# Kernel tuning notes

Measured on AMD Instinct MI355X. Metric: run time of the kernel, lower is better.

Reference implementation:

```python
import jax, jax.numpy as jnp
import numpy as np

B, T, N = 256, 50, 32          # graphs per batch, timesteps, nodes per scene graph
FIN, HG, HR, HFC = 16, 64, 64, 128  # gnn in, gnn hidden, gnn out (== HG, shared LayerNorm), gru hidden
DS, DTG, OST, OCA = 32, 32, 8, 8    # sensor dim, target dim, stimuli classes, cause classes


def _ln(x, g, b, eps=1e-5):
    m = jnp.mean(x, axis=-1, keepdims=True)
    v = jnp.var(x, axis=-1, keepdims=True)
    return (x - m) * jax.lax.rsqrt(v + eps) * g + b


def _gru_seq(x, Wi, Wh, bi, bh):
    # x: [B, T, Din] -> [B, T, H]; PyTorch GRU gate order (r, z, n)
    xp = x @ Wi + bi  # precompute input projections for all timesteps
    H = Wh.shape[0]
    h0 = jnp.zeros((x.shape[0], H), x.dtype)
    def step(h, xt):
        gh = h @ Wh + bh
        ir, iz, ig = jnp.split(xt, 3, axis=-1)
        hr, hz, hg = jnp.split(gh, 3, axis=-1)
        r = jax.nn.sigmoid(ir + hr)
        z = jax.nn.sigmoid(iz + hz)
        n = jnp.tanh(ig + r * hg)
        hn = (1.0 - z) * n + z * h
        return hn, hn
    _, ys = jax.lax.scan(step, h0, jnp.swapaxes(xp, 0, 1))
    return jnp.swapaxes(ys, 0, 1)


def _glorot(key, shape):
    s = jnp.sqrt(2.0 / (shape[0] + shape[-1]))
    return jax.random.normal(key, shape, jnp.float32) * s


def setup_inputs() -> dict:
    key = jax.random.key(0)
    ks = jax.random.split(key, 24)
    inp = {
        'feat': jax.random.normal(ks[0], (B, T, N, FIN), jnp.float32),
        'sensor': jax.random.normal(ks[1], (B, T, DS), jnp.float32),
        'target': jax.random.normal(ks[2], (B, T, DTG), jnp.float32),
        'adj': jax.random.randint(ks[3], (B, T, N, N), 0, 2, jnp.int32),
        'W_g1': _glorot(ks[4], (FIN, HG)), 'b_g1': jnp.zeros((HG,)),
        'W_g3': _glorot(ks[5], (HG, HR)), 'b_g3': jnp.zeros((HR,)),
        'ln_g_g': jnp.ones((HG,)), 'ln_g_b': jnp.zeros((HG,)),
    }
    for i, (sfx, din) in enumerate([('G', HR), ('S', DS), ('T', DTG)]):
        inp['Wi' + sfx] = _glorot(ks[6 + 2 * i], (din, 3 * HFC))
        inp['Wh' + sfx] = _glorot(ks[7 + 2 * i], (HFC, 3 * HFC))
        inp['bi' + sfx] = jnp.zeros((3 * HFC,))
        inp['bh' + sfx] = jnp.zeros((3 * HFC,))
    inp['W_fc1'] = _glorot(ks[12], (3 * HFC, HFC)); inp['b_fc1'] = jnp.zeros((HFC,))
    inp['ln_fc_g'] = jnp.ones((HFC,)); inp['ln_fc_b'] = jnp.zeros((HFC,))
    inp['W_st'] = _glorot(ks[13], (HFC, OST)); inp['b_st'] = jnp.zeros((OST,))
    inp['W_ca'] = _glorot(ks[14], (HFC, OCA)); inp['b_ca'] = jnp.zeros((OCA,))
    return inp


def reference(feat, sensor, target, W_g1, b_g1, W_g3, b_g3, ln_g_g, ln_g_b,
              WiG, WhG, biG, bhG, WiS, WhS, biS, bhS, WiT, WhT, biT, bhT,
              W_fc1, b_fc1, ln_fc_g, ln_fc_b, W_st, b_st, W_ca, b_ca, adj):
    # Batched mean-aggregation GNN (self-loops avoid zero in-degree), fused over all B*T graphs.
    adj_f = adj.astype(jnp.float32) + jnp.eye(N, dtype=jnp.float32)
    deg = jnp.sum(adj_f, axis=-1, keepdims=True)  # [B,T,N,1]
    def gnn(h, W, b):
        agg = jnp.einsum('btij,btjf->btif', adj_f, h) / deg
        return jax.nn.relu(_ln(agg @ W + b, ln_g_g, ln_g_b))  # linear -> norm -> relu (dropout=0)
    h1 = gnn(feat, W_g1, b_g1)   # gnn1c
    h2 = gnn(h1, W_g3, b_g3)     # gnn3c
    graph_seq = h2[:, :, 0, :]   # hG[0]: node-0 readout per (graph, timestep) -> [B,T,HR]
    gG = _gru_seq(graph_seq, WiG, WhG, biG, bhG)
    gS = _gru_seq(sensor, WiS, WhS, biS, bhS)
    gT = _gru_seq(target, WiT, WhT, biT, bhT)
    out = jnp.concatenate([gG, gS, gT], axis=-1).reshape(-1, 3 * HFC)  # [B*T, 384]
    h = jax.nn.relu(_ln(out @ W_fc1 + b_fc1, ln_fc_g, ln_fc_b))
    return (h @ W_st + b_st, h @ W_ca + b_ca)
```

## Files before the change

kernel.cpp:

```cpp
#include <hip/hip_runtime.h>
#include <stdint.h>

typedef unsigned short u16;

#define DI __device__ __forceinline__

DI float b2f(u16 u){ union{ unsigned int i; float f; } v; v.i = ((unsigned int)u)<<16; return v.f; }
DI u16 f2bf(float f){ union{ float f; unsigned int u; } v; v.f = f;
  unsigned int u = v.u; return (u16)((u + 0x7FFFu + ((u>>16)&1u)) >> 16); }
DI float ubf_lo(unsigned w){ union{ unsigned u; float f; } v; v.u = w<<16; return v.f; }
DI float ubf_hi(unsigned w){ union{ unsigned u; float f; } v; v.u = w & 0xFFFF0000u; return v.f; }
DI float sigm_(float x){ return 1.0f/(1.0f + __expf(-x)); }
DI float tanh_(float x){ x = fminf(fmaxf(x,-15.0f),15.0f); float e = __expf(2.0f*x); return (e-1.0f)/(e+1.0f); }

DI bool probe_bf(const void* ones){ return ((const u16*)ones)[0] == 0x3F80u; }

template<bool BF>
DI float ld(const void* p, long i){
  if constexpr (BF) return b2f(((const u16*)p)[i]);
  else              return ((const float*)p)[i];
}

#if defined(__has_builtin)
#if __has_builtin(__builtin_amdgcn_fdot2)
#define F16DOT 1
#endif
#endif
#ifndef F16DOT
#define F16DOT 0
#endif

#if F16DOT
typedef _Float16 f16x2 __attribute__((ext_vector_type(2)));
DI unsigned pk2(float lo, float hi){
  union{ f16x2 h; unsigned u; } v;
  v.h[0] = (_Float16)lo; v.h[1] = (_Float16)hi;
  return v.u;
}
DI float dot2(unsigned w, unsigned x, float c){
  union{ unsigned u; f16x2 h; } a, b;
  a.u = w; b.u = x;
  return __builtin_amdgcn_fdot2(a.h, b.h, c, false);
}
DI u16 cvt1(float v){ union{ _Float16 h; u16 u; } c; c.h = (_Float16)v; return c.u; }
#else
DI unsigned pk2(float lo, float hi){
  return (unsigned)f2bf(lo) | ((unsigned)f2bf(hi)<<16);
}
DI float dot2(unsigned w, unsigned x, float c){
  return c + ubf_lo(w)*ubf_lo(x) + ubf_hi(w)*ubf_hi(x);
}
DI u16 cvt1(float v){ return f2bf(v); }
#endif

constexpr int T_ = 50;
constexpr int BT = 256*50;

template<bool BF>
__global__ __launch_bounds__(256) void k_gnn(
    const int* __restrict__ adj, const void* __restrict__ feat,
    const void* __restrict__ Wg1, const void* __restrict__ bg1,
    const void* __restrict__ Wg3, const void* __restrict__ bg3,
    const void* __restrict__ lng, const void* __restrict__ lnb,
    u16* __restrict__ gs)
{
  if(probe_bf(lng) != BF) return;

  __shared__ __align__(16) float s_adj[32*36];
  __shared__ float s_dinv[32];
  __shared__ __align__(16) float s_featT[16*36];
  __shared__ float s_b1[64], s_b3[64], s_lg[64], s_lb[64];
  __shared__ __align__(16) float s_ag1[32*20];
  __shared__ __align__(16) float s_z1[32*68];
  __shared__ float s_m[32], s_r[32];

  float* s_p2 = s_featT;
  float* s_q2 = s_ag1;

  const int tid = threadIdx.x;
  const long bt = blockIdx.x;

  float w1c[16];
  float wg3r[16];
  {
    int o = tid&63, fg = tid>>6;
    #pragma unroll
    for(int f=0; f<16; f++)
      w1c[f] = ld<BF>(Wg1, f*64 + o);
    #pragma unroll
    for(int ff=0; ff<16; ff++)
      wg3r[ff] = ld<BF>(Wg3, (fg*16+ff)*64 + o);
  }

  {
    const int4* ap4 = (const int4*)(adj + bt*1024);
    int4 v = ap4[tid];
    int i = tid>>3, j0 = (tid&7)*4;
    float4 f4;
    f4.x = (float)v.x + (i==j0   ? 1.0f : 0.0f);
    f4.y = (float)v.y + (i==j0+1 ? 1.0f : 0.0f);
    f4.z = (float)v.z + (i==j0+2 ? 1.0f : 0.0f);
    f4.w = (float)v.w + (i==j0+3 ? 1.0f : 0.0f);
    *(float4*)&s_adj[i*36+j0] = f4;

    for(int idx=tid; idx<512; idx+=256){
      int r = idx>>4, f = idx&15;
      s_featT[f*36+r] = ld<BF>(feat, bt*512 + idx);
    }
    if(tid<64){ s_b1[tid]=ld<BF>(bg1,tid); s_b3[tid]=ld<BF>(bg3,tid);
                s_lg[tid]=ld<BF>(lng,tid); s_lb[tid]=ld<BF>(lnb,tid); }
  }
  __syncthreads();

  #pragma unroll
  for(int rep=0; rep<2; rep++){
    int idx = tid + rep*256;
    int i = idx>>4, f = idx&15;
    const float4* ar = (const float4*)(s_adj + i*36);
    const float4* fr = (const float4*)(s_featT + f*36);
    float4 acc = {0.f,0.f,0.f,0.f};
    #pragma unroll
    for(int k=0;k<8;k++){
      float4 a = ar[k], b = fr[k];
      acc.x += a.x*b.x; acc.y += a.y*b.y; acc.z += a.z*b.z; acc.w += a.w*b.w;
    }
    s_ag1[i*20+f] = (acc.x+acc.y)+(acc.z+acc.w);
  }
  if(tid<32){
    const float4* ar = (const float4*)(s_adj + tid*36);
    float4 s4 = {0.f,0.f,0.f,0.f};
    #pragma unroll
    for(int k=0;k<8;k++){
      float4 a = ar[k];
      s4.x += a.x; s4.y += a.y; s4.z += a.z; s4.w += a.w;
    }
    s_dinv[tid] = 1.0f/((s4.x+s4.y)+(s4.z+s4.w));
  }
  __syncthreads();

  #pragma unroll
  for(int rep=0; rep<8; rep++){
    int idx = tid + rep*256;
    int i = idx>>6, o = idx&63;
    const float4* ag = (const float4*)(s_ag1 + i*20);
    float4 a0 = ag[0], a1 = ag[1], a2 = ag[2], a3 = ag[3];
    float acc0 = a0.x*w1c[0] + a0.y*w1c[1] + a0.z*w1c[2] + a0.w*w1c[3];
    float acc1 = a1.x*w1c[4] + a1.y*w1c[5] + a1.z*w1c[6] + a1.w*w1c[7];
    float acc2 = a2.x*w1c[8] + a2.y*w1c[9] + a2.z*w1c[10]+ a2.w*w1c[11];
    float acc3 = a3.x*w1c[12]+ a3.y*w1c[13]+ a3.z*w1c[14]+ a3.w*w1c[15];
    s_z1[i*68+o] = ((acc0+acc1)+(acc2+acc3))*s_dinv[i] + s_b1[o];
  }
  __syncthreads();

  if(tid<32){
    const float4* zr = (const float4*)(s_z1 + tid*68);
    float4 s4={0.f,0.f,0.f,0.f}, q4={0.f,0.f,0.f,0.f};
    #pragma unroll
    for(int k=0;k<16;k++){
      float4 v = zr[k];
      s4.x+=v.x; s4.y+=v.y; s4.z+=v.z; s4.w+=v.w;
      q4.x+=v.x*v.x; q4.y+=v.y*v.y; q4.z+=v.z*v.z; q4.w+=v.w*v.w;
    }
    float s = (s4.x+s4.y)+(s4.z+s4.w);
    float q = (q4.x+q4.y)+(q4.z+q4.w);
    float m = s*(1.0f/64.0f);
    float var = q*(1.0f/64.0f) - m*m;
    s_m[tid]=m; s_r[tid]=rsqrtf(var + 1e-5f);
  }
  __syncthreads();

  {
    int o = tid&63, jg = tid>>6;
    float lg_o = s_lg[o], lb_o = s_lb[o];
    float s=0.f;
    #pragma unroll
    for(int jj=0;jj<8;jj++){
      int j = jg*8+jj;
      float h = fmaxf((s_z1[j*68+o]-s_m[j])*s_r[j]*lg_o + lb_o, 0.0f);
      s += s_adj[j]*h;
    }
    s_p2[jg*64+o] = s;
  }
  __syncthreads();

  {
    int o = tid&63, fg = tid>>6;
    float dinv0 = s_dinv[0];
    float acc=0.f;
    #pragma unroll
    for(int ff=0;ff<16;ff++){
      int f = fg*16+ff;
      float a2f = (s_p2[f]+s_p2[64+f]+s_p2[128+f]+s_p2[192+f])*dinv0;
      acc += a2f*wg3r[ff];
    }
    s_q2[fg*64+o] = acc;
  }
  __syncthreads();

  if(tid<64){
    float z = s_q2[tid]+s_q2[64+tid]+s_q2[128+tid]+s_q2[192+tid] + s_b3[tid];
    s_p2[tid] = z;
    s_q2[tid] = z*z;
    #pragma unroll
    for(int off=32; off>=1; off>>=1){
      if(tid<off){ s_p2[tid]+=s_p2[tid+off]; s_q2[tid]+=s_q2[tid+off]; }
    }
    float m = s_p2[0]*(1.0f/64.0f);
    float var = s_q2[0]*(1.0f/64.0f) - m*m;
    float r = rsqrtf(var+1e-5f);
    float v = (z-m)*r*s_lg[tid] + s_lb[tid];
    gs[bt*64+tid] = f2bf(fmaxf(v,0.0f));
  }
}

template<bool BF>
__global__ __launch_bounds__(384, 3) void k_gru_f(
    const u16* __restrict__ gs,
    const void* __restrict__ sen, const void* __restrict__ tgt,
    const void* __restrict__ WiG, const void* __restrict__ biG,
    const void* __restrict__ WiS, const void* __restrict__ biS,
    const void* __restrict__ WiT, const void* __restrict__ biT,
    const void* __restrict__ WhG, const void* __restrict__ bhG,
    const void* __restrict__ WhS, const void* __restrict__ bhS,
    const void* __restrict__ WhT, const void* __restrict__ bhT,
    const void* __restrict__ probe, u16* __restrict__ gout)
{
  if(probe_bf(probe) != BF) return;

  __shared__ __align__(4) u16 s_xp[T_*384];
  __shared__ __align__(16) unsigned s_x[T_*32];
  __shared__ __align__(16) u16 s_hu[128];
  __shared__ float s_r[128], s_z[128];

  const int tid = threadIdx.x;
  const int g = blockIdx.y;
  const long row = blockIdx.x;
  const void* Wi = (g==0)?WiG:((g==1)?WiS:WiT);
  const void* bi = (g==0)?biG:((g==1)?biS:biT);
  const void* Wh = (g==0)?WhG:((g==1)?WhS:WhT);
  const void* bh = (g==0)?bhG:((g==1)?bhS:bhT);
  const int din = (g==0)?64:32;
  const int kmax = din>>1;

  unsigned wi2[32];
  #pragma unroll
  for(int k2=0;k2<32;k2++){
    if(k2<kmax){
      float lo = ld<BF>(Wi,(long)(2*k2  )*384+tid);
      float hi = ld<BF>(Wi,(long)(2*k2+1)*384+tid);
      wi2[k2] = pk2(lo,hi);
    } else wi2[k2] = 0u;
  }
  #pragma unroll
  for(int k2=0;k2<32;k2++) asm volatile("" : "+v"(wi2[k2]));

  const float bi_t = ld<BF>(bi,tid);
  const float bh_t = ld<BF>(bh,tid);

  if(g==0){
    const unsigned* xr = (const unsigned*)(gs + row*(T_*64));
    for(int idx=tid; idx<T_*32; idx+=384){
      unsigned w = xr[idx];
      s_x[idx] = pk2(ubf_lo(w), ubf_hi(w));
    }
  } else {
    const void* src = (g==1)?sen:tgt;
    const long base0 = (long)row*(T_*32);
    for(int idx=tid; idx<T_*16; idx+=384){
      float lo = ld<BF>(src, base0 + 2*idx);
      float hi = ld<BF>(src, base0 + 2*idx+1);
      s_x[idx] = pk2(lo,hi);
    }
  }
  if(tid<64) ((unsigned*)s_hu)[tid] = 0u;
  __syncthreads();

  if(g==0){
    const uint4* x4 = (const uint4*)s_x;
    for(int t=0;t<T_;t++){
      float a0=0.f,a1=0.f,a2=0.f,a3=0.f;
      #pragma unroll
      for(int q=0;q<8;q++){
        uint4 xv = x4[t*8+q];
        a0 = dot2(wi2[4*q+0], xv.x, a0);
        a1 = dot2(wi2[4*q+1], xv.y, a1);
        a2 = dot2(wi2[4*q+2], xv.z, a2);
        a3 = dot2(wi2[4*q+3], xv.w, a3);
      }
      s_xp[t*384+tid] = f2bf(((a0+a1)+(a2+a3)) + bi_t);
    }
  } else {
    const uint4* x4 = (const uint4*)s_x;
    for(int t=0;t<T_;t++){
      float a0=0.f,a1=0.f,a2=0.f,a3=0.f;
      #pragma unroll
      for(int q=0;q<4;q++){
        uint4 xv = x4[t*4+q];
        a0 = dot2(wi2[4*q+0], xv.x, a0);
        a1 = dot2(wi2[4*q+1], xv.y, a1);
        a2 = dot2(wi2[4*q+2], xv.z, a2);
        a3 = dot2(wi2[4*q+3], xv.w, a3);
      }
      s_xp[t*384+tid] = f2bf(((a0+a1)+(a2+a3)) + bi_t);
    }
  }

  unsigned whh[64];
  #pragma unroll
  for(int k2=0;k2<64;k2++){
    float lo = ld<BF>(Wh,(long)(2*k2  )*384+tid);
    float hi = ld<BF>(Wh,(long)(2*k2+1)*384+tid);
    whh[k2] = pk2(lo,hi);
  }
  #pragma unroll
  for(int k2=0;k2<64;k2++) asm volatile("" : "+v"(whh[k2]));
  __syncthreads();

  const int seg = tid>>7, j = tid&127;
  float h_own = 0.f;

  for(int t=0;t<T_;t++){
    const uint4* h4 = (const uint4*)s_hu;
    float a0=0.f,a1=0.f,a2=0.f,a3=0.f;
    #pragma unroll
    for(int q=0;q<16;q++){
      uint4 hv = h4[q];
      a0 = dot2(whh[4*q+0], hv.x, a0);
      a1 = dot2(whh[4*q+1], hv.y, a1);
      a2 = dot2(whh[4*q+2], hv.z, a2);
      a3 = dot2(whh[4*q+3], hv.w, a3);
    }
    float gh = ((a0+a1)+(a2+a3)) + bh_t;
    float xp_own = b2f(s_xp[t*384+tid]);
    if(seg==0)      s_r[j] = sigm_(xp_own + gh);
    else if(seg==1) s_z[j] = sigm_(xp_own + gh);
    __syncthreads();
    if(seg==2){
      float r = s_r[j], z = s_z[j];
      float n = tanh_(xp_own + r*gh);
      float hn = (1.0f-z)*n + z*h_own;
      h_own = hn;
      s_hu[j] = cvt1(hn);
      s_xp[t*384+j] = f2bf(hn);
    }
    __syncthreads();
  }

  u16* go = gout + ((long)g*BT + row*T_)*128;
  const unsigned* sx32 = (const unsigned*)s_xp;
  unsigned* go32 = (unsigned*)go;
  for(int idx2=tid; idx2<3200; idx2+=384){
    int e0 = idx2*2;
    int t = e0>>7, jj = e0&127;
    go32[(t*128+jj)>>1] = sx32[(t*384+jj)>>1];
  }
}

template<bool BF>
__global__ __launch_bounds__(256) void k_head(
    const u16* __restrict__ gout,
    const void* __restrict__ Wfc, const void* __restrict__ bfc,
    const void* __restrict__ lg, const void* __restrict__ lb,
    const void* __restrict__ Wst, const void* __restrict__ bst,
    const void* __restrict__ Wca, const void* __restrict__ bca,
    void* __restrict__ out)
{
  if(probe_bf(lg) != BF) return;

  __shared__ __align__(16) float s_oT[384*8];
  __shared__ __align__(16) float s_z[8*132];
  __shared__ __align__(16) float s_h[8*132];
  __shared__ float s_mr[16];
  const int tid=threadIdx.x;
  const long r0 = (long)blockIdx.x*8;

  for(int idx=tid; idx<8*384; idx+=256){
    int r = idx/384, c = idx - r*384;
    int seg = c>>7, j = c&127;
    s_oT[c*8+r] = b2f(gout[(long)seg*BT*128 + (r0+r)*128 + j]);
  }
  __syncthreads();

  const int o = tid&127, rs = tid>>7;
  float acc[4]={0,0,0,0};
  for(int k=0;k<384;k++){
    float wv = ld<BF>(Wfc, (long)k*128+o);
    float4 hv = *(const float4*)&s_oT[k*8 + rs*4];
    acc[0] += hv.x*wv; acc[1] += hv.y*wv; acc[2] += hv.z*wv; acc[3] += hv.w*wv;
  }
  float bv = ld<BF>(bfc,o);
  #pragma unroll
  for(int rr=0;rr<4;rr++) s_z[(rs*4+rr)*132 + o] = acc[rr] + bv;
  __syncthreads();

  if(tid<8){
    const float4* zr = (const float4*)(s_z + tid*132);
    float4 s4={0.f,0.f,0.f,0.f}, q4={0.f,0.f,0.f,0.f};
    #pragma unroll
    for(int k=0;k<32;k++){
      float4 v = zr[k];
      s4.x+=v.x; s4.y+=v.y; s4.z+=v.z; s4.w+=v.w;
      q4.x+=v.x*v.x; q4.y+=v.y*v.y; q4.z+=v.z*v.z; q4.w+=v.w*v.w;
    }
    float s = (s4.x+s4.y)+(s4.z+s4.w);
    float qq = (q4.x+q4.y)+(q4.z+q4.w);
    float m=s*(1.0f/128.0f), var=qq*(1.0f/128.0f)-m*m;
    s_mr[tid]=m; s_mr[8+tid]=rsqrtf(var+1e-5f);
  }
  __syncthreads();

  #pragma unroll
  for(int rep=0; rep<4; rep++){
    int idx = tid + rep*256;
    int r = idx>>7, j = idx&127;
    float v = (s_z[r*132+j]-s_mr[r])*s_mr[8+r]*ld<BF>(lg,j) + ld<BF>(lb,j);
    s_h[r*132+j]=fmaxf(v,0.f);
  }
  __syncthreads();

  if(tid<128){
    int r = tid>>4, oo = tid&15;
    int which = oo>>3, oc = oo&7;
    const void* W = which? Wca : Wst;
    const void* bb = which? bca : bst;
    float s=0.f;
    for(int k=0;k<128;k++) s += s_h[r*132+k]*ld<BF>(W,(long)k*8+oc);
    s += ld<BF>(bb,oc);
    long pos = (long)which*BT*8 + (r0+r)*8 + oc;
    if constexpr (BF) ((u16*)out)[pos]  = f2bf(s);
    else              ((float*)out)[pos] = s;
  }
}

extern "C" void kernel_launch(void* const* d_in, const int* in_sizes, int n_in,
                              void* d_out, int out_size, void* d_ws, size_t ws_size,
                              hipStream_t stream)
{
  const void* feat  = d_in[0];
  const void* sen   = d_in[1];
  const void* tgt   = d_in[2];
  const int*  adj   = (const int*)d_in[3];
  const void* Wg1   = d_in[4];
  const void* bg1   = d_in[5];
  const void* Wg3   = d_in[6];
  const void* bg3   = d_in[7];
  const void* lng   = d_in[8];
  const void* lnb   = d_in[9];
  const void* WiG   = d_in[10];
  const void* WhG   = d_in[11];
  const void* biG   = d_in[12];
  const void* bhG   = d_in[13];
  const void* WiS   = d_in[14];
  const void* WhS   = d_in[15];
  const void* biS   = d_in[16];
  const void* bhS   = d_in[17];
  const void* WiT   = d_in[18];
  const void* WhT   = d_in[19];
  const void* biT   = d_in[20];
  const void* bhT   = d_in[21];
  const void* Wfc   = d_in[22];
  const void* bfc   = d_in[23];
  const void* lfg   = d_in[24];
  const void* lfb   = d_in[25];
  const void* Wst   = d_in[26];
  const void* bst   = d_in[27];
  const void* Wca   = d_in[28];
  const void* bca   = d_in[29];

  u16* gs = (u16*)d_ws;
  u16* go = gs + (long)BT*64;

  k_gnn<true ><<<dim3(BT), dim3(256), 0, stream>>>(adj, feat, Wg1, bg1, Wg3, bg3, lng, lnb, gs);
  k_gnn<false><<<dim3(BT), dim3(256), 0, stream>>>(adj, feat, Wg1, bg1, Wg3, bg3, lng, lnb, gs);

  k_gru_f<true ><<<dim3(256,3), dim3(384), 0, stream>>>(gs, sen, tgt,
      WiG, biG, WiS, biS, WiT, biT, WhG, bhG, WhS, bhS, WhT, bhT, lng, go);
  k_gru_f<false><<<dim3(256,3), dim3(384), 0, stream>>>(gs, sen, tgt,
      WiG, biG, WiS, biS, WiT, biT, WhG, bhG, WhS, bhS, WhT, bhT, lng, go);

  k_head<true ><<<dim3(BT/8), dim3(256), 0, stream>>>(go, Wfc, bfc, lfg, lfb, Wst, bst, Wca, bca, d_out);
  k_head<false><<<dim3(BT/8), dim3(256), 0, stream>>>(go, Wfc, bfc, lfg, lfb, Wst, bst, Wca, bca, d_out);
}
```

Before: 408.9 us.

## Process four sequences per GRU block and fuse input projection into recurrence

```diff
diff --git a/kernel.cpp b/kernel.cpp
--- a/kernel.cpp
+++ b/kernel.cpp
@@ -214,7 +214,7 @@
 }
 
 template<bool BF>
-__global__ __launch_bounds__(384, 3) void k_gru_f(
+__global__ __launch_bounds__(384, 1) void k_gru_f(
     const u16* __restrict__ gs,
     const void* __restrict__ sen, const void* __restrict__ tgt,
     const void* __restrict__ WiG, const void* __restrict__ biG,
@@ -227,132 +227,127 @@
 {
   if(probe_bf(probe) != BF) return;
 
-  __shared__ __align__(4) u16 s_xp[T_*384];
-  __shared__ __align__(16) unsigned s_x[T_*32];
-  __shared__ __align__(16) u16 s_hu[128];
-  __shared__ float s_r[128], s_z[128];
+  __shared__ __align__(16) unsigned s_x[4*50*32];
+  __shared__ __align__(16) u16 s_hu[4][128];
+  __shared__ float s_r[4][128], s_z[4][128];
 
   const int tid = threadIdx.x;
   const int g = blockIdx.y;
-  const long row = blockIdx.x;
+  const int row0 = blockIdx.x*4;
   const void* Wi = (g==0)?WiG:((g==1)?WiS:WiT);
   const void* bi = (g==0)?biG:((g==1)?biS:biT);
   const void* Wh = (g==0)?WhG:((g==1)?WhS:WhT);
   const void* bh = (g==0)?bhG:((g==1)?bhS:bhT);
-  const int din = (g==0)?64:32;
-  const int kmax = din>>1;
-
-  unsigned wi2[32];
-  #pragma unroll
-  for(int k2=0;k2<32;k2++){
-    if(k2<kmax){
-      float lo = ld<BF>(Wi,(long)(2*k2  )*384+tid);
-      float hi = ld<BF>(Wi,(long)(2*k2+1)*384+tid);
-      wi2[k2] = pk2(lo,hi);
-    } else wi2[k2] = 0u;
-  }
-  #pragma unroll
-  for(int k2=0;k2<32;k2++) asm volatile("" : "+v"(wi2[k2]));
+  const int kmax = (g==0)?32:16;
+
+  unsigned whc[64];
+  #pragma unroll
+  for(int k2=0;k2<64;k2++)
+    whc[k2] = pk2(ld<BF>(Wh,(long)(2*k2  )*384+tid),
+                  ld<BF>(Wh,(long)(2*k2+1)*384+tid));
+  unsigned wic[32];
+  #pragma unroll
+  for(int k2=0;k2<32;k2++)
+    wic[k2] = (k2<kmax)? pk2(ld<BF>(Wi,(long)(2*k2  )*384+tid),
+                             ld<BF>(Wi,(long)(2*k2+1)*384+tid)) : 0u;
+  #pragma unroll
+  for(int k2=0;k2<64;k2++) asm volatile("" : "+v"(whc[k2]));
+  #pragma unroll
+  for(int k2=0;k2<32;k2++) asm volatile("" : "+v"(wic[k2]));
 
   const float bi_t = ld<BF>(bi,tid);
   const float bh_t = ld<BF>(bh,tid);
 
   if(g==0){
-    const unsigned* xr = (const unsigned*)(gs + row*(T_*64));
-    for(int idx=tid; idx<T_*32; idx+=384){
-      unsigned w = xr[idx];
+    const unsigned* xr = (const unsigned*)gs;
+    for(int idx=tid; idx<4*50*32; idx+=384){
+      int rr = idx/1600, rem = idx - rr*1600;
+      unsigned w = xr[(long)(row0+rr)*1600 + rem];
       s_x[idx] = pk2(ubf_lo(w), ubf_hi(w));
     }
   } else {
     const void* src = (g==1)?sen:tgt;
-    const long base0 = (long)row*(T_*32);
-    for(int idx=tid; idx<T_*16; idx+=384){
-      float lo = ld<BF>(src, base0 + 2*idx);
-      float hi = ld<BF>(src, base0 + 2*idx+1);
-      s_x[idx] = pk2(lo,hi);
-    }
-  }
-  if(tid<64) ((unsigned*)s_hu)[tid] = 0u;
-  __syncthreads();
-
-  if(g==0){
-    const uint4* x4 = (const uint4*)s_x;
-    for(int t=0;t<T_;t++){
+    for(int idx=tid; idx<4*50*16; idx+=384){
+      int rr = idx/800, rem = idx - rr*800;
+      int t = rem>>4, k2 = rem&15;
+      long base = ((long)(row0+rr)*50 + t)*32 + 2*k2;
+      s_x[(rr*50+t)*32 + k2] = pk2(ld<BF>(src,base), ld<BF>(src,base+1));
+    }
+  }
+  for(int idx=tid; idx<256; idx+=384) ((unsigned*)s_hu)[idx] = 0u;
+  __syncthreads();
+
+  const int seg = tid>>7, j = tid&127;
+  float h_own[4] = {0.f,0.f,0.f,0.f};
+  u16* gouw = gout + (long)g*BT*128;
+
+  for(int t=0;t<T_;t++){
+    float gh[4], xp[4];
+    #pragma unroll
+    for(int rr=0;rr<4;rr++){
+      const uint4* h4 = (const uint4*)s_hu[rr];
       float a0=0.f,a1=0.f,a2=0.f,a3=0.f;
       #pragma unroll
-      for(int q=0;q<8;q++){
-        uint4 xv = x4[t*8+q];
-        a0 = dot2(wi2[4*q+0], xv.x, a0);
-        a1 = dot2(wi2[4*q+1], xv.y, a1);
-        a2 = dot2(wi2[4*q+2], xv.z, a2);
-        a3 = dot2(wi2[4*q+3], xv.w, a3);
+      for(int q=0;q<16;q++){
+        uint4 hv = h4[q];
+        a0 = dot2(whc[4*q+0], hv.x, a0);
+        a1 = dot2(whc[4*q+1], hv.y, a1);
+        a2 = dot2(whc[4*q+2], hv.z, a2);
+        a3 = dot2(whc[4*q+3], hv.w, a3);
       }
-      s_xp[t*384+tid] = f2bf(((a0+a1)+(a2+a3)) + bi_t);
-    }
-  } else {
-    const uint4* x4 = (const uint4*)s_x;
-    for(int t=0;t<T_;t++){
-      float a0=0.f,a1=0.f,a2=0.f,a3=0.f;
-      #pragma unroll
-      for(int q=0;q<4;q++){
-        uint4 xv = x4[t*4+q];
-        a0 = dot2(wi2[4*q+0], xv.x, a0);
-        a1 = dot2(wi2[4*q+1], xv.y, a1);
-        a2 = dot2(wi2[4*q+2], xv.z, a2);
-        a3 = dot2(wi2[4*q+3], xv.w, a3);
+      gh[rr] = ((a0+a1)+(a2+a3)) + bh_t;
+    }
+    if(g==0){
+      #pragma unroll
+      for(int rr=0;rr<4;rr++){
+        const uint4* x4 = (const uint4*)&s_x[(rr*50+t)*32];
+        float a0=0.f,a1=0.f,a2=0.f,a3=0.f;
+        #pragma unroll
+        for(int q=0;q<8;q++){
+          uint4 xv = x4[q];
+          a0 = dot2(wic[4*q+0], xv.x, a0);
+          a1 = dot2(wic[4*q+1], xv.y, a1);
+          a2 = dot2(wic[4*q+2], xv.z, a2);
+          a3 = dot2(wic[4*q+3], xv.w, a3);
+        }
+        xp[rr] = ((a0+a1)+(a2+a3)) + bi_t;
       }
-      s_xp[t*384+tid] = f2bf(((a0+a1)+(a2+a3)) + bi_t);
-    }
-  }
-
-  unsigned whh[64];
-  #pragma unroll
-  for(int k2=0;k2<64;k2++){
-    float lo = ld<BF>(Wh,(long)(2*k2  )*384+tid);
-    float hi = ld<BF>(Wh,(long)(2*k2+1)*384+tid);
-    whh[k2] = pk2(lo,hi);
-  }
-  #pragma unroll
-  for(int k2=0;k2<64;k2++) asm volatile("" : "+v"(whh[k2]));
-  __syncthreads();
-
-  const int seg = tid>>7, j = tid&127;
-  float h_own = 0.f;
-
-  for(int t=0;t<T_;t++){
-    const uint4* h4 = (const uint4*)s_hu;
-    float a0=0.f,a1=0.f,a2=0.f,a3=0.f;
-    #pragma unroll
-    for(int q=0;q<16;q++){
-      uint4 hv = h4[q];
-      a0 = dot2(whh[4*q+0], hv.x, a0);
-      a1 = dot2(whh[4*q+1], hv.y, a1);
-      a2 = dot2(whh[4*q+2], hv.z, a2);
-      a3 = dot2(whh[4*q+3], hv.w, a3);
-    }
-    float gh = ((a0+a1)+(a2+a3)) + bh_t;
-    float xp_own = b2f(s_xp[t*384+tid]);
-    if(seg==0)      s_r[j] = sigm_(xp_own + gh);
-    else if(seg==1) s_z[j] = sigm_(xp_own + gh);
+    } else {
+      #pragma unroll
+      for(int rr=0;rr<4;rr++){
+        const uint4* x4 = (const uint4*)&s_x[(rr*50+t)*32];
+        float a0=0.f,a1=0.f,a2=0.f,a3=0.f;
+        #pragma unroll
+        for(int q=0;q<4;q++){
+          uint4 xv = x4[q];
+          a0 = dot2(wic[4*q+0], xv.x, a0);
+          a1 = dot2(wic[4*q+1], xv.y, a1);
+          a2 = dot2(wic[4*q+2], xv.z, a2);
+          a3 = dot2(wic[4*q+3], xv.w, a3);
+        }
+        xp[rr] = ((a0+a1)+(a2+a3)) + bi_t;
+      }
+    }
+    if(seg==0){
+      #pragma unroll
+      for(int rr=0;rr<4;rr++) s_r[rr][j] = sigm_(xp[rr] + gh[rr]);
+    } else if(seg==1){
+      #pragma unroll
+      for(int rr=0;rr<4;rr++) s_z[rr][j] = sigm_(xp[rr] + gh[rr]);
+    }
     __syncthreads();
     if(seg==2){
-      float r = s_r[j], z = s_z[j];
-      float n = tanh_(xp_own + r*gh);
-      float hn = (1.0f-z)*n + z*h_own;
-      h_own = hn;
-      s_hu[j] = cvt1(hn);
-      s_xp[t*384+j] = f2bf(hn);
+      #pragma unroll
+      for(int rr=0;rr<4;rr++){
+        float r = s_r[rr][j], z = s_z[rr][j];
+        float n = tanh_(xp[rr] + r*gh[rr]);
+        float hn = (1.0f-z)*n + z*h_own[rr];
+        h_own[rr] = hn;
+        s_hu[rr][j] = cvt1(hn);
+        gouw[((long)(row0+rr)*T_ + t)*128 + j] = f2bf(hn);
+      }
     }
     __syncthreads();
-  }
-
-  u16* go = gout + ((long)g*BT + row*T_)*128;
-  const unsigned* sx32 = (const unsigned*)s_xp;
-  unsigned* go32 = (unsigned*)go;
-  for(int idx2=tid; idx2<3200; idx2+=384){
-    int e0 = idx2*2;
-    int t = e0>>7, jj = e0&127;
-    go32[(t*128+jj)>>1] = sx32[(t*384+jj)>>1];
   }
 }
 
@@ -473,9 +468,9 @@
   k_gnn<true ><<<dim3(BT), dim3(256), 0, stream>>>(adj, feat, Wg1, bg1, Wg3, bg3, lng, lnb, gs);
   k_gnn<false><<<dim3(BT), dim3(256), 0, stream>>>(adj, feat, Wg1, bg1, Wg3, bg3, lng, lnb, gs);
 
-  k_gru_f<true ><<<dim3(256,3), dim3(384), 0, stream>>>(gs, sen, tgt,
+  k_gru_f<true ><<<dim3(64,3), dim3(384), 0, stream>>>(gs, sen, tgt,
       WiG, biG, WiS, biS, WiT, biT, WhG, bhG, WhS, bhS, WhT, bhT, lng, go);
-  k_gru_f<false><<<dim3(256,3), dim3(384), 0, stream>>>(gs, sen, tgt,
+  k_gru_f<false><<<dim3(64,3), dim3(384), 0, stream>>>(gs, sen, tgt,
       WiG, biG, WiS, biS, WiT, biT, WhG, bhG, WhS, bhS, WhT, bhT, lng, go);
 
   k_head<true ><<<dim3(BT/8), dim3(256), 0, stream>>>(go, Wfc, bfc, lfg, lfb, Wst, bst, Wca, bca, d_out);
```

Measured after the change: 1.076 ms. +163.1%, slower.
